# Performance work log

Measured on AMD Instinct MI355X. Metric: run time of the kernel, lower is better.

The kernel has to match this reference:

```python
import jax, jax.numpy as jnp
import numpy as np

B, S, D = 2, 2048, 2048
NH, NKV = 32, 8
HD = D // NH          # 64
NREP = NH // NKV      # 4


def _rope(x, cos, sin):
    # x: [B, S, H, HD]; cos/sin: [S, HD//2]
    x2 = x.reshape(*x.shape[:-1], HD // 2, 2)
    x0, x1 = x2[..., 0], x2[..., 1]
    c = cos[None, :, None, :]
    s = sin[None, :, None, :]
    r0 = x0 * c - x1 * s
    r1 = x0 * s + x1 * c
    return jnp.stack([r0, r1], axis=-1).reshape(x.shape)


def setup_inputs() -> dict:
    key = jax.random.key(0)
    ks = jax.random.split(key, 5)
    x = jax.random.normal(ks[0], (B, S, D), dtype=jnp.float32)
    wq = jax.random.normal(ks[1], (D, NH * HD), dtype=jnp.float32) * (D ** -0.5)
    wk = jax.random.normal(ks[2], (D, NKV * HD), dtype=jnp.float32) * (D ** -0.5)
    wv = jax.random.normal(ks[3], (D, NKV * HD), dtype=jnp.float32) * (D ** -0.5)
    wo = jax.random.normal(ks[4], (NH * HD, D), dtype=jnp.float32) * (D ** -0.5)
    # standard RoPE frequencies: theta = 10000^(-2i/HD)
    inv_freq = 1.0 / (10000.0 ** (np.arange(0, HD, 2, dtype=np.float32) / HD))
    angles = np.arange(S, dtype=np.float32)[:, None] * inv_freq[None, :]  # [S, HD/2]
    freqs_cos = jnp.asarray(np.cos(angles))
    freqs_sin = jnp.asarray(np.sin(angles))
    return {"x": x, "freqs_cos": freqs_cos, "freqs_sin": freqs_sin,
            "wq": wq, "wk": wk, "wv": wv, "wo": wo}


def reference(x, freqs_cos, freqs_sin, wq, wk, wv, wo):
    b, s, _ = x.shape
    xq = (x @ wq).reshape(b, s, NH, HD)
    xk = (x @ wk).reshape(b, s, NKV, HD)
    xv = (x @ wv).reshape(b, s, NKV, HD)
    xq = _rope(xq, freqs_cos, freqs_sin)
    xk = _rope(xk, freqs_cos, freqs_sin)
    # GQA repeat_kv: expand kv heads to NH
    keys = jnp.repeat(xk, NREP, axis=2)    # [B, S, NH, HD]
    values = jnp.repeat(xv, NREP, axis=2)
    scores = jnp.einsum('bqhd,bkhd->bhqk', xq, keys) / jnp.sqrt(jnp.float32(HD))
    causal = jnp.tril(jnp.ones((s, s), dtype=bool))
    scores = jnp.where(causal[None, None], scores, -jnp.inf)
    attn = jax.nn.softmax(scores.astype(jnp.float32), axis=-1).astype(xq.dtype)
    out = jnp.einsum('bhqk,bkhd->bqhd', attn, values).reshape(b, s, NH * HD)
    return out @ wo
```

## Files before the change

### kernel.cpp

```cpp
#include <hip/hip_runtime.h>
#include <hip/hip_bf16.h>

#define S_LEN 2048
#define DMODEL 2048
#define N_H 32
#define N_KV 8
#define H_D 64
#define ROWS 4096
#define QKV_LD 3072

typedef __bf16 bf16x8 __attribute__((ext_vector_type(8)));
typedef float f32x4 __attribute__((ext_vector_type(4)));

static __device__ __forceinline__ unsigned short f2bf(float f) {
  unsigned int u = __float_as_uint(f);
  u += 0x7FFFu + ((u >> 16) & 1u);
  return (unsigned short)(u >> 16);
}
static __device__ __forceinline__ float bf2f(unsigned short s) {
  return __uint_as_float((unsigned int)s << 16);
}

static __device__ __forceinline__ void async16(const void* g, void* l) {
  __builtin_amdgcn_global_load_lds(
      (const __attribute__((address_space(1))) unsigned int*)g,
      (__attribute__((address_space(3))) unsigned int*)l, 16, 0, 0);
}

__global__ __launch_bounds__(256) void cvt_bf16_k(
    const float* __restrict__ in, unsigned short* __restrict__ out) {
  const size_t i = ((size_t)blockIdx.x * 256 + threadIdx.x) * 8;
  const float4 a = *(const float4*)&in[i];
  const float4 b = *(const float4*)&in[i + 4];
  union { unsigned short u[8]; uint4 v; } p;
  p.u[0] = f2bf(a.x); p.u[1] = f2bf(a.y); p.u[2] = f2bf(a.z); p.u[3] = f2bf(a.w);
  p.u[4] = f2bf(b.x); p.u[5] = f2bf(b.y); p.u[6] = f2bf(b.z); p.u[7] = f2bf(b.w);
  *(uint4*)&out[i] = p.v;
}

__global__ __launch_bounds__(256) void prep_all_k(
    const float* __restrict__ x, const float* __restrict__ wq,
    const float* __restrict__ wk, const float* __restrict__ wv,
    const float* __restrict__ wo, unsigned short* __restrict__ xb,
    unsigned short* __restrict__ wqkvT, unsigned short* __restrict__ woT) {
  const int z = blockIdx.z;
  if (z == 4) {
    const size_t i =
        (((size_t)blockIdx.y * 64 + blockIdx.x) * 256 + threadIdx.x) * 8;
    const float4 a = *(const float4*)&x[i];
    const float4 b = *(const float4*)&x[i + 4];
    union { unsigned short u[8]; uint4 v; } p;
    p.u[0] = f2bf(a.x); p.u[1] = f2bf(a.y); p.u[2] = f2bf(a.z); p.u[3] = f2bf(a.w);
    p.u[4] = f2bf(b.x); p.u[5] = f2bf(b.y); p.u[6] = f2bf(b.z); p.u[7] = f2bf(b.w);
    *(uint4*)&xb[i] = p.v;
    return;
  }
  const float* in;
  unsigned short* out;
  int C;
  if (z == 0)      { in = wq; out = wqkvT;                  C = 2048; }
  else if (z == 1) { in = wk; out = wqkvT + 2048ull * 2048; C = 512;  }
  else if (z == 2) { in = wv; out = wqkvT + 2560ull * 2048; C = 512;  }
  else             { in = wo; out = woT;                    C = 2048; }
  if (blockIdx.x * 32 >= C) return;

  __shared__ unsigned short tile[32][33];
  const int tx = threadIdx.x & 31;
  const int ty = threadIdx.x >> 5;
  const int r0 = blockIdx.y * 32;
  const int c0 = blockIdx.x * 32;
#pragma unroll
  for (int i = 0; i < 32; i += 8)
    tile[ty + i][tx] = f2bf(in[(size_t)(r0 + ty + i) * C + c0 + tx]);
  __syncthreads();
#pragma unroll
  for (int i = 0; i < 32; i += 8)
    out[(size_t)(c0 + ty + i) * 2048 + r0 + tx] = tile[tx][ty + i];
}

#define SCALE_LOG2E 0.18033688011112042f

__global__ __launch_bounds__(256) void rope_vt_k(
    unsigned short* __restrict__ qkv, unsigned short* __restrict__ vT,
    const float* __restrict__ fc, const float* __restrict__ fs) {
  const int blk = blockIdx.x;
  if (blk < 20480) {
    const int PQ = ROWS * N_H * (H_D / 2);
    const int PK = ROWS * N_KV * (H_D / 2);
    const int idx = blk * 256 + threadIdx.x;
    if (idx >= PQ + PK) return;
    unsigned short* base;
    float c, sn;
    bool isq;
    if (idx < PQ) {
      const int i = idx & 31;
      const int h = (idx >> 5) & 31;
      const int row = idx >> 10;
      const int s = row & (S_LEN - 1);
      c = fc[s * 32 + i];
      sn = fs[s * 32 + i];
      base = qkv + (size_t)row * QKV_LD + h * H_D + 2 * i;
      isq = true;
    } else {
      const int p = idx - PQ;
      const int i = p & 31;
      const int h = (p >> 5) & 7;
      const int row = p >> 8;
      const int s = row & (S_LEN - 1);
      c = fc[s * 32 + i];
      sn = fs[s * 32 + i];
      base = qkv + (size_t)row * QKV_LD + 2048 + h * H_D + 2 * i;
      isq = false;
    }
    const float x0 = bf2f(base[0]);
    const float x1 = bf2f(base[1]);
    const float sc = isq ? SCALE_LOG2E : 1.0f;
    base[0] = f2bf((x0 * c - x1 * sn) * sc);
    base[1] = f2bf((x0 * sn + x1 * c) * sc);
  } else {
    __shared__ unsigned short tile[32][33];
    const int t = blk - 20480;
    const int bx = t & 15;
    const int by = t >> 4;
    const unsigned short* in = qkv + 2560;
    const int tx = threadIdx.x & 31;
    const int ty = threadIdx.x >> 5;
    const int r0 = by * 32;
    const int c0 = bx * 32;
#pragma unroll
    for (int i = 0; i < 32; i += 8)
      tile[ty + i][tx] = in[(size_t)(r0 + ty + i) * QKV_LD + c0 + tx];
    __syncthreads();
#pragma unroll
    for (int i = 0; i < 32; i += 8)
      vT[(size_t)(c0 + ty + i) * ROWS + r0 + tx] = tile[tx][ty + i];
  }
}

template <int STORE_BF16>
__global__ __launch_bounds__(256) void gemm_bt_k(
    const unsigned short* __restrict__ A, const unsigned short* __restrict__ BT,
    void* __restrict__ Cp, int M, int N, int K, int lda) {
  __shared__ __align__(16) unsigned short As[128 * 32];
  __shared__ __align__(16) unsigned short Bs[128 * 32];
  const int tid = threadIdx.x;
  const int wave = tid >> 6;
  const int lane = tid & 63;
  const int quad = lane >> 4;
  const int l16 = lane & 15;
  const int m0 = blockIdx.x * 128;
  const int n0 = blockIdx.y * 128;
  const int wm = (wave >> 1) * 64;
  const int wn = (wave & 1) * 64;
  const int rsub = lane >> 2;
  const int coff = (lane & 3) * 8;
  f32x4 acc[4][4] = {};

  for (int kt = 0; kt < K; kt += 32) {
    __syncthreads();
#pragma unroll
    for (int t = 0; t < 2; t++) {
      const int row = wave * 32 + t * 16 + rsub;
      async16(&A[(size_t)(m0 + row) * lda + kt + coff],
              &As[(wave * 32 + t * 16) * 32]);
      async16(&BT[(size_t)(n0 + row) * K + kt + coff],
              &Bs[(wave * 32 + t * 16) * 32]);
    }
    __syncthreads();
    bf16x8 af[4], bfr[4];
#pragma unroll
    for (int i = 0; i < 4; i++)
      af[i] = *(const bf16x8*)&As[(wm + i * 16 + l16) * 32 + quad * 8];
#pragma unroll
    for (int j = 0; j < 4; j++)
      bfr[j] = *(const bf16x8*)&Bs[(wn + j * 16 + l16) * 32 + quad * 8];
#pragma unroll
    for (int i = 0; i < 4; i++)
#pragma unroll
      for (int j = 0; j < 4; j++)
        acc[i][j] =
            __builtin_amdgcn_mfma_f32_16x16x32_bf16(af[i], bfr[j], acc[i][j], 0, 0, 0);
  }

#pragma unroll
  for (int i = 0; i < 4; i++) {
#pragma unroll
    for (int e = 0; e < 4; e++) {
      const int mrow = m0 + wm + i * 16 + quad * 4 + e;
#pragma unroll
      for (int j = 0; j < 4; j++) {
        const int ncol = n0 + wn + j * 16 + l16;
        const float val = acc[i][j][e];
        if (STORE_BF16) {
          ((unsigned short*)Cp)[(size_t)mrow * N + ncol] = f2bf(val);
        } else {
          ((float*)Cp)[(size_t)mrow * N + ncol] = val;
        }
      }
    }
  }
}

template <int AF32, int STORE_BF16>
__global__ __launch_bounds__(256) void gemm_k(
    const void* __restrict__ Ap, const float* __restrict__ B,
    void* __restrict__ Cp, int M, int N, int K) {
  constexpr int LDP = 40;
  __shared__ __align__(16) unsigned short As[128 * LDP];
  __shared__ __align__(16) unsigned short Bs[128 * LDP];
  const int tid = threadIdx.x;
  const int wave = tid >> 6;
  const int lane = tid & 63;
  const int quad = lane >> 4;
  const int l16 = lane & 15;
  const int m0 = blockIdx.x * 128;
  const int n0 = blockIdx.y * 128;
  const int wm = (wave >> 1) * 64;
  const int wn = (wave & 1) * 64;
  f32x4 acc[4][4] = {};

  for (int kt = 0; kt < K; kt += 32) {
    __syncthreads();
    if (AF32) {
      const float* A = (const float*)Ap;
      for (int c = tid; c < 1024; c += 256) {
        const int r = c >> 3;
        const int cc = (c & 7) << 2;
        const float4 w = *(const float4*)&A[(size_t)(m0 + r) * K + kt + cc];
        union { unsigned short u[4]; uint2 v; } p;
        p.u[0] = f2bf(w.x); p.u[1] = f2bf(w.y);
        p.u[2] = f2bf(w.z); p.u[3] = f2bf(w.w);
        *(uint2*)&As[r * LDP + cc] = p.v;
      }
    } else {
      const unsigned short* A = (const unsigned short*)Ap;
      for (int c = tid; c < 512; c += 256) {
        const int r = c >> 2;
        const int cc = (c & 3) << 3;
        *(uint4*)&As[r * LDP + cc] =
            *(const uint4*)&A[(size_t)(m0 + r) * K + kt + cc];
      }
    }
    for (int c = tid; c < 1024; c += 256) {
      const int kr = c >> 5;
      const int nc = (c & 31) << 2;
      const float4 w = *(const float4*)&B[(size_t)(kt + kr) * N + n0 + nc];
      Bs[(nc + 0) * LDP + kr] = f2bf(w.x);
      Bs[(nc + 1) * LDP + kr] = f2bf(w.y);
      Bs[(nc + 2) * LDP + kr] = f2bf(w.z);
      Bs[(nc + 3) * LDP + kr] = f2bf(w.w);
    }
    __syncthreads();
    bf16x8 af[4], bfr[4];
#pragma unroll
    for (int i = 0; i < 4; i++)
      af[i] = *(const bf16x8*)&As[(wm + i * 16 + l16) * LDP + quad * 8];
#pragma unroll
    for (int j = 0; j < 4; j++)
      bfr[j] = *(const bf16x8*)&Bs[(wn + j * 16 + l16) * LDP + quad * 8];
#pragma unroll
    for (int i = 0; i < 4; i++)
#pragma unroll
      for (int j = 0; j < 4; j++)
        acc[i][j] =
            __builtin_amdgcn_mfma_f32_16x16x32_bf16(af[i], bfr[j], acc[i][j], 0, 0, 0);
  }
#pragma unroll
  for (int i = 0; i < 4; i++) {
#pragma unroll
    for (int e = 0; e < 4; e++) {
      const int mrow = m0 + wm + i * 16 + quad * 4 + e;
#pragma unroll
      for (int j = 0; j < 4; j++) {
        const int ncol = n0 + wn + j * 16 + l16;
        const float val = acc[i][j][e];
        if (STORE_BF16) {
          ((unsigned short*)Cp)[(size_t)mrow * N + ncol] = f2bf(val);
        } else {
          ((float*)Cp)[(size_t)mrow * N + ncol] = val;
        }
      }
    }
  }
}

__global__ __launch_bounds__(256) void rope_k(
    unsigned short* __restrict__ q, unsigned short* __restrict__ kk,
    const float* __restrict__ fc, const float* __restrict__ fs,
    int qstride, int kstride) {
  const int PQ = ROWS * N_H * (H_D / 2);
  const int PK = ROWS * N_KV * (H_D / 2);
  const int idx = blockIdx.x * 256 + threadIdx.x;
  if (idx >= PQ + PK) return;
  unsigned short* base;
  float c, sn;
  if (idx < PQ) {
    const int i = idx & 31;
    const int h = (idx >> 5) & 31;
    const int row = idx >> 10;
    const int s = row & (S_LEN - 1);
    c = fc[s * 32 + i];
    sn = fs[s * 32 + i];
    base = q + (size_t)row * qstride + h * H_D + 2 * i;
  } else {
    const int p = idx - PQ;
    const int i = p & 31;
    const int h = (p >> 5) & 7;
    const int row = p >> 8;
    const int s = row & (S_LEN - 1);
    c = fc[s * 32 + i];
    sn = fs[s * 32 + i];
    base = kk + (size_t)row * kstride + h * H_D + 2 * i;
  }
  const float x0 = bf2f(base[0]);
  const float x1 = bf2f(base[1]);
  base[0] = f2bf(x0 * c - x1 * sn);
  base[1] = f2bf(x0 * sn + x1 * c);
}

__global__ __launch_bounds__(512, 2) void attn_mfma9_k(
    const unsigned short* __restrict__ qkv, const unsigned short* __restrict__ vT,
    unsigned short* __restrict__ ao) {
  const int pair = blockIdx.x, h = blockIdx.y, b = blockIdx.z;
  const int hk = h >> 2;
  const int tid = threadIdx.x;
  const int wave = tid >> 6;
  const int l16 = tid & 15;
  const int quad = (tid & 63) >> 4;
  const int rr = tid >> 3;
  const int dc = (tid & 7) * 8;
  const int rx = (l16 & 7) << 3;
  const int sx = (rr & 7) << 3;

  __shared__ __align__(16) unsigned short Ks[2][64 * 64];
  __shared__ __align__(16) unsigned short Vt[2][64 * 64];
  __shared__ __align__(16) unsigned short Ps[8][32 * 64];

  bf16x8 ones;
#pragma unroll
  for (int j = 0; j < 8; j++) ones[j] = (__bf16)1.0f;

  const size_t kbase =
      (size_t)(b * S_LEN) * QKV_LD + 2048 + hk * H_D + dc;
  const size_t vbase = (size_t)(hk * H_D + rr) * ROWS + b * S_LEN + dc;

  for (int sel = 0; sel < 2; ++sel) {
    const int qb = sel ? (7 - pair) : pair;
    const int row0 = qb * 256;
    const int ktiles = 4 * qb + 4;

    bf16x8 af[2][2];
#pragma unroll
    for (int r = 0; r < 2; r++) {
      const size_t qrow =
          (size_t)(b * S_LEN + row0 + wave * 32 + r * 16 + l16);
#pragma unroll
      for (int c = 0; c < 2; c++)
        af[r][c] =
            *(const bf16x8*)&qkv[qrow * QKV_LD + h * H_D + c * 32 + quad * 8];
    }

    f32x4 o_acc[2][4] = {};
    f32x4 l_acc[2] = {};

    uint4 rk, rv;
    rk = *(const uint4*)&qkv[kbase + (size_t)rr * QKV_LD];
    rv = *(const uint4*)&vT[vbase];
    __syncthreads();
    *(uint4*)&Ks[0][rr * 64 + (dc ^ sx)] = rk;
    *(uint4*)&Vt[0][rr * 64 + (dc ^ sx)] = rv;

    for (int kt = 0; kt < ktiles; kt += 2) {
#pragma unroll
      for (int half = 0; half < 2; ++half) {
        const int kcur = kt + half;
        if (kcur + 1 < ktiles) {
          rk = *(const uint4*)&qkv[kbase +
                                   (size_t)((kcur + 1) * 64 + rr) * QKV_LD];
          rv = *(const uint4*)&vT[vbase + (size_t)(kcur + 1) * 64];
        }
        __syncthreads();

        f32x4 sacc[2][4];
#pragma unroll
        for (int n = 0; n < 4; n++) {
          f32x4 z0 = {}, z1 = {};
#pragma unroll
          for (int c = 0; c < 2; c++) {
            const bf16x8 bk =
                *(const bf16x8*)&Ks[half][(n * 16 + l16) * 64 +
                                          ((c * 32 + quad * 8) ^ rx)];
            z0 = __builtin_amdgcn_mfma_f32_16x16x32_bf16(bk, af[0][c], z0, 0, 0, 0);
            z1 = __builtin_amdgcn_mfma_f32_16x16x32_bf16(bk, af[1][c], z1, 0, 0, 0);
          }
          sacc[0][n] = z0;
          sacc[1][n] = z1;
        }

        const bool maybe_mask = (kcur >= 4 * qb);
        const int krel0 = (kcur - 4 * qb) * 64;
#pragma unroll
        for (int r = 0; r < 2; r++) {
          const int qn = wave * 32 + r * 16 + l16;
          const int prow = (r * 16 + l16) * 64;
#pragma unroll
          for (int n = 0; n < 4; n++) {
            const int kb0 = krel0 + n * 16 + quad * 4;
            float pe[4];
#pragma unroll
            for (int e = 0; e < 4; e++) {
              float v = exp2f(sacc[r][n][e]);
              if (maybe_mask && (kb0 + e > qn)) v = 0.f;
              pe[e] = v;
            }
            uint2 u;
            u.x = __builtin_amdgcn_perm(__float_as_uint(pe[1]),
                                        __float_as_uint(pe[0]), 0x07060302u);
            u.y = __builtin_amdgcn_perm(__float_as_uint(pe[3]),
                                        __float_as_uint(pe[2]), 0x07060302u);
            *(uint2*)&Ps[wave][prow + ((n * 16 + quad * 4) ^ rx)] = u;
          }
        }

        bf16x8 pf[2][2];
#pragma unroll
        for (int r = 0; r < 2; r++)
#pragma unroll
          for (int c = 0; c < 2; c++)
            pf[r][c] = *(const bf16x8*)&Ps[wave][(r * 16 + l16) * 64 +
                                                ((c * 32 + quad * 8) ^ rx)];
#pragma unroll
        for (int c = 0; c < 2; c++) {
          l_acc[0] = __builtin_amdgcn_mfma_f32_16x16x32_bf16(pf[0][c], ones,
                                                             l_acc[0], 0, 0, 0);
          l_acc[1] = __builtin_amdgcn_mfma_f32_16x16x32_bf16(pf[1][c], ones,
                                                             l_acc[1], 0, 0, 0);
        }
#pragma unroll
        for (int n = 0; n < 4; n++)
#pragma unroll
          for (int c = 0; c < 2; c++) {
            const bf16x8 bv =
                *(const bf16x8*)&Vt[half][(n * 16 + l16) * 64 +
                                          ((c * 32 + quad * 8) ^ rx)];
            o_acc[0][n] = __builtin_amdgcn_mfma_f32_16x16x32_bf16(
                pf[0][c], bv, o_acc[0][n], 0, 0, 0);
            o_acc[1][n] = __builtin_amdgcn_mfma_f32_16x16x32_bf16(
                pf[1][c], bv, o_acc[1][n], 0, 0, 0);
          }

        if (kcur + 1 < ktiles) {
          *(uint4*)&Ks[half ^ 1][rr * 64 + (dc ^ sx)] = rk;
          *(uint4*)&Vt[half ^ 1][rr * 64 + (dc ^ sx)] = rv;
        }
      }
    }

#pragma unroll
    for (int r = 0; r < 2; r++)
#pragma unroll
      for (int e = 0; e < 4; e++) {
        const float inv = 1.f / l_acc[r][e];
        const size_t row =
            (size_t)(b * S_LEN + row0 + wave * 32 + r * 16 + quad * 4 + e);
#pragma unroll
        for (int n = 0; n < 4; n++)
          ao[row * QKV_LD + h * H_D + n * 16 + l16] = f2bf(o_acc[r][n][e] * inv);
      }
  }
}

#define LK 72

__global__ __launch_bounds__(256) void attn_mfma_k(
    const unsigned short* __restrict__ q, const unsigned short* __restrict__ k,
    const unsigned short* __restrict__ v, unsigned short* __restrict__ ao) {
  const int qt = blockIdx.x, h = blockIdx.y, b = blockIdx.z;
  const int hk = h >> 2;
  const int tid = threadIdx.x;
  const int wave = tid >> 6;
  const int l16 = tid & 15;
  const int quad = (tid & 63) >> 4;

  __shared__ __align__(16) unsigned short Ks[64 * LK];
  __shared__ __align__(16) unsigned short Vt[64 * LK];
  __shared__ __align__(16) unsigned short Ps[64 * LK];

  bf16x8 af[2];
  {
    const size_t qrow = (size_t)(b * S_LEN + qt * 64 + wave * 16 + l16);
#pragma unroll
    for (int c = 0; c < 2; c++)
      af[c] = *(const bf16x8*)&q[qrow * DMODEL + h * H_D + c * 32 + quad * 8];
  }

  f32x4 o_acc[4] = {};
  float m_i[4], l_i[4];
#pragma unroll
  for (int e = 0; e < 4; e++) { m_i[e] = -INFINITY; l_i[e] = 0.f; }

  for (int kt = 0; kt <= qt; ++kt) {
    const int kb = kt * 64;
    __syncthreads();
    {
      const int kr = tid >> 2;
      const int dc = (tid & 3) * 16;
      const size_t gro = (size_t)(b * S_LEN + kb + kr) * (N_KV * H_D) + hk * H_D + dc;
      *(uint4*)&Ks[kr * LK + dc] = *(const uint4*)&k[gro];
      *(uint4*)&Ks[kr * LK + dc + 8] = *(const uint4*)&k[gro + 8];
      union { unsigned short u[8]; uint4 v; } w0, w1;
      w0.v = *(const uint4*)&v[gro];
      w1.v = *(const uint4*)&v[gro + 8];
#pragma unroll
      for (int j = 0; j < 8; j++) Vt[(dc + j) * LK + kr] = w0.u[j];
#pragma unroll
      for (int j = 0; j < 8; j++) Vt[(dc + 8 + j) * LK + kr] = w1.u[j];
    }
    __syncthreads();

    f32x4 sacc[4];
#pragma unroll
    for (int n = 0; n < 4; n++) {
      f32x4 z = {};
#pragma unroll
      for (int c = 0; c < 2; c++) {
        const bf16x8 bk = *(const bf16x8*)&Ks[(n * 16 + l16) * LK + c * 32 + quad * 8];
        z = __builtin_amdgcn_mfma_f32_16x16x32_bf16(af[c], bk, z, 0, 0, 0);
      }
      sacc[n] = z;
    }

    float p[4][4], mnew[4];
#pragma unroll
    for (int e = 0; e < 4; e++) mnew[e] = m_i[e];
#pragma unroll
    for (int n = 0; n < 4; n++)
#pragma unroll
      for (int e = 0; e < 4; e++) {
        float s = sacc[n][e] * 0.125f;
        if (kt == qt && (n * 16 + l16) > (wave * 16 + quad * 4 + e))
          s = -INFINITY;
        p[n][e] = s;
        mnew[e] = fmaxf(mnew[e], s);
      }
#pragma unroll
    for (int e = 0; e < 4; e++) {
      mnew[e] = fmaxf(mnew[e], __shfl_xor(mnew[e], 1));
      mnew[e] = fmaxf(mnew[e], __shfl_xor(mnew[e], 2));
      mnew[e] = fmaxf(mnew[e], __shfl_xor(mnew[e], 4));
      mnew[e] = fmaxf(mnew[e], __shfl_xor(mnew[e], 8));
      const float alpha = __expf(m_i[e] - mnew[e]);
      m_i[e] = mnew[e];
      l_i[e] *= alpha;
#pragma unroll
      for (int n = 0; n < 4; n++) o_acc[n][e] *= alpha;
    }
#pragma unroll
    for (int n = 0; n < 4; n++)
#pragma unroll
      for (int e = 0; e < 4; e++) {
        const float pe = __expf(p[n][e] - m_i[e]);
        p[n][e] = pe;
        l_i[e] += pe;
      }

#pragma unroll
    for (int n = 0; n < 4; n++)
#pragma unroll
      for (int e = 0; e < 4; e++)
        Ps[(wave * 16 + quad * 4 + e) * LK + n * 16 + l16] = f2bf(p[n][e]);
    __syncthreads();

    bf16x8 pf[2];
#pragma unroll
    for (int c = 0; c < 2; c++)
      pf[c] = *(const bf16x8*)&Ps[(wave * 16 + l16) * LK + c * 32 + quad * 8];
#pragma unroll
    for (int n = 0; n < 4; n++)
#pragma unroll
      for (int c = 0; c < 2; c++) {
        const bf16x8 bv = *(const bf16x8*)&Vt[(n * 16 + l16) * LK + c * 32 + quad * 8];
        o_acc[n] = __builtin_amdgcn_mfma_f32_16x16x32_bf16(pf[c], bv, o_acc[n], 0, 0, 0);
      }
  }

#pragma unroll
  for (int e = 0; e < 4; e++) {
    l_i[e] += __shfl_xor(l_i[e], 1);
    l_i[e] += __shfl_xor(l_i[e], 2);
    l_i[e] += __shfl_xor(l_i[e], 4);
    l_i[e] += __shfl_xor(l_i[e], 8);
    const float inv = 1.f / l_i[e];
    const size_t row = (size_t)(b * S_LEN + qt * 64 + wave * 16 + quad * 4 + e);
#pragma unroll
    for (int n = 0; n < 4; n++)
      ao[row * DMODEL + h * H_D + n * 16 + l16] = f2bf(o_acc[n][e] * inv);
  }
}

extern "C" void kernel_launch(void* const* d_in, const int* in_sizes, int n_in,
                              void* d_out, int out_size, void* d_ws, size_t ws_size,
                              hipStream_t stream) {
  const float* x = (const float*)d_in[0];
  const float* fc = (const float*)d_in[1];
  const float* fs = (const float*)d_in[2];
  const float* wq = (const float*)d_in[3];
  const float* wk = (const float*)d_in[4];
  const float* wv = (const float*)d_in[5];
  const float* wo = (const float*)d_in[6];

  char* ws = (char*)d_ws;
  const dim3 b256(256);

  if (ws_size >= (64ull << 20)) {
    unsigned short* qkv = (unsigned short*)(ws);
    unsigned short* xb = (unsigned short*)(ws + (24ull << 20));
    unsigned short* wqkvT = (unsigned short*)(ws + (40ull << 20));
    unsigned short* woT = (unsigned short*)(ws + (52ull << 20));
    unsigned short* vT = (unsigned short*)(ws + (60ull << 20));

    prep_all_k<<<dim3(64, 64, 5), b256, 0, stream>>>(x, wq, wk, wv, wo, xb,
                                                     wqkvT, woT);

    gemm_bt_k<1><<<dim3(32, 24), b256, 0, stream>>>(xb, wqkvT, qkv, 4096, 3072,
                                                    2048, 2048);

    rope_vt_k<<<dim3(20480 + 2048), b256, 0, stream>>>(qkv, vT, fc, fs);

    attn_mfma9_k<<<dim3(4, N_H, 2), dim3(512), 0, stream>>>(qkv, vT, qkv);

    gemm_bt_k<0><<<dim3(32, 16), b256, 0, stream>>>(qkv, woT, d_out, 4096, 2048,
                                                    2048, QKV_LD);
  } else {
    unsigned short* q = (unsigned short*)(ws);
    unsigned short* k = (unsigned short*)(ws + (16ull << 20));
    unsigned short* v = (unsigned short*)(ws + (20ull << 20));
    unsigned short* xb = (unsigned short*)(ws + (24ull << 20));
    const bool have_xb = ws_size >= (40ull << 20);

    if (have_xb) {
      cvt_bf16_k<<<dim3(ROWS * DMODEL / (256 * 8)), b256, 0, stream>>>(x, xb);
      gemm_k<0, 1><<<dim3(32, 16), b256, 0, stream>>>(xb, wq, q, 4096, 2048, 2048);
      gemm_k<0, 1><<<dim3(32, 4), b256, 0, stream>>>(xb, wk, k, 4096, 512, 2048);
      gemm_k<0, 1><<<dim3(32, 4), b256, 0, stream>>>(xb, wv, v, 4096, 512, 2048);
    } else {
      gemm_k<1, 1><<<dim3(32, 16), b256, 0, stream>>>(x, wq, q, 4096, 2048, 2048);
      gemm_k<1, 1><<<dim3(32, 4), b256, 0, stream>>>(x, wk, k, 4096, 512, 2048);
      gemm_k<1, 1><<<dim3(32, 4), b256, 0, stream>>>(x, wv, v, 4096, 512, 2048);
    }

    rope_k<<<dim3(20480), b256, 0, stream>>>(q, k, fc, fs, N_H * H_D, N_KV * H_D);
    attn_mfma_k<<<dim3(S_LEN / 64, N_H, 2), b256, 0, stream>>>(q, k, v, q);
    gemm_k<0, 0><<<dim3(32, 16), b256, 0, stream>>>(q, wo, d_out, 4096, 2048, 2048);
  }
}
```

Before: 324.4 us.

## Split attention key tiles across two wave groups with LDS reduction

The attention kernel now processes 128-row query blocks with two groups of four waves. Each group handles alternate 64-key tiles from the same query rows, and the partial outputs and row sums are combined through shared memory at the end. The grid doubles to 8 pairs per head and the launch bound is raised to 4 blocks per CU, aiming for more parallelism and better load balance in the causal loop. In exchange it adds an extra cross-group reduction and more barriers, and an odd-length tail is avoided only because the tile count is always even.

```diff
diff --git a/kernel.cpp b/kernel.cpp
--- a/kernel.cpp
+++ b/kernel.cpp
@@ -318,13 +318,16 @@
   base[1] = f2bf(x0 * sn + x1 * c);
 }
 
-__global__ __launch_bounds__(512, 2) void attn_mfma9_k(
+__global__ __launch_bounds__(512, 4) void attn_mfma10_k(
     const unsigned short* __restrict__ qkv, const unsigned short* __restrict__ vT,
     unsigned short* __restrict__ ao) {
   const int pair = blockIdx.x, h = blockIdx.y, b = blockIdx.z;
   const int hk = h >> 2;
   const int tid = threadIdx.x;
   const int wave = tid >> 6;
+  const int g = wave >> 2;
+  const int w4 = wave & 3;
+  const int lane = tid & 63;
   const int l16 = tid & 15;
   const int quad = (tid & 63) >> 4;
   const int rr = tid >> 3;
@@ -336,6 +339,12 @@
   __shared__ __align__(16) unsigned short Vt[2][64 * 64];
   __shared__ __align__(16) unsigned short Ps[8][32 * 64];
 
+  const unsigned short* Kb = &Ks[g][0];
+  const unsigned short* Vb = &Vt[g][0];
+
+  f32x4* Ored = (f32x4*)&Ps[0][0];
+  f32x4* Lred = (f32x4*)&Ks[0][0];
+
   bf16x8 ones;
 #pragma unroll
   for (int j = 0; j < 8; j++) ones[j] = (__bf16)1.0f;
@@ -345,15 +354,15 @@
   const size_t vbase = (size_t)(hk * H_D + rr) * ROWS + b * S_LEN + dc;
 
   for (int sel = 0; sel < 2; ++sel) {
-    const int qb = sel ? (7 - pair) : pair;
-    const int row0 = qb * 256;
-    const int ktiles = 4 * qb + 4;
+    const int qb = sel ? (15 - pair) : pair;
+    const int row0 = qb * 128;
+    const int ktiles = 2 * qb + 2;
 
     bf16x8 af[2][2];
 #pragma unroll
     for (int r = 0; r < 2; r++) {
       const size_t qrow =
-          (size_t)(b * S_LEN + row0 + wave * 32 + r * 16 + l16);
+          (size_t)(b * S_LEN + row0 + w4 * 32 + r * 16 + l16);
 #pragma unroll
       for (int c = 0; c < 2; c++)
         af[r][c] =
@@ -363,110 +372,134 @@
     f32x4 o_acc[2][4] = {};
     f32x4 l_acc[2] = {};
 
-    uint4 rk, rv;
-    rk = *(const uint4*)&qkv[kbase + (size_t)rr * QKV_LD];
-    rv = *(const uint4*)&vT[vbase];
-    __syncthreads();
-    *(uint4*)&Ks[0][rr * 64 + (dc ^ sx)] = rk;
-    *(uint4*)&Vt[0][rr * 64 + (dc ^ sx)] = rv;
+    uint4 rk0, rk1, rv0, rv1;
+    rk0 = *(const uint4*)&qkv[kbase + (size_t)(0 * 64 + rr) * QKV_LD];
+    rk1 = *(const uint4*)&qkv[kbase + (size_t)(1 * 64 + rr) * QKV_LD];
+    rv0 = *(const uint4*)&vT[vbase + (size_t)0 * 64];
+    rv1 = *(const uint4*)&vT[vbase + (size_t)1 * 64];
+    __syncthreads();
+    *(uint4*)&Ks[0][rr * 64 + (dc ^ sx)] = rk0;
+    *(uint4*)&Ks[1][rr * 64 + (dc ^ sx)] = rk1;
+    *(uint4*)&Vt[0][rr * 64 + (dc ^ sx)] = rv0;
+    *(uint4*)&Vt[1][rr * 64 + (dc ^ sx)] = rv1;
 
     for (int kt = 0; kt < ktiles; kt += 2) {
-#pragma unroll
-      for (int half = 0; half < 2; ++half) {
-        const int kcur = kt + half;
-        if (kcur + 1 < ktiles) {
-          rk = *(const uint4*)&qkv[kbase +
-                                   (size_t)((kcur + 1) * 64 + rr) * QKV_LD];
-          rv = *(const uint4*)&vT[vbase + (size_t)(kcur + 1) * 64];
+      if (kt + 2 < ktiles) {
+        rk0 = *(const uint4*)&qkv[kbase + (size_t)((kt + 2) * 64 + rr) * QKV_LD];
+        rk1 = *(const uint4*)&qkv[kbase + (size_t)((kt + 3) * 64 + rr) * QKV_LD];
+        rv0 = *(const uint4*)&vT[vbase + (size_t)(kt + 2) * 64];
+        rv1 = *(const uint4*)&vT[vbase + (size_t)(kt + 3) * 64];
+      }
+      __syncthreads();
+
+      const int kcur = kt + g;
+
+      f32x4 sacc[2][4];
+#pragma unroll
+      for (int n = 0; n < 4; n++) {
+        f32x4 z0 = {}, z1 = {};
+#pragma unroll
+        for (int c = 0; c < 2; c++) {
+          const bf16x8 bk = *(const bf16x8*)&Kb[(n * 16 + l16) * 64 +
+                                               ((c * 32 + quad * 8) ^ rx)];
+          z0 = __builtin_amdgcn_mfma_f32_16x16x32_bf16(bk, af[0][c], z0, 0, 0, 0);
+          z1 = __builtin_amdgcn_mfma_f32_16x16x32_bf16(bk, af[1][c], z1, 0, 0, 0);
         }
-        __syncthreads();
-
-        f32x4 sacc[2][4];
+        sacc[0][n] = z0;
+        sacc[1][n] = z1;
+      }
+
+      const bool maybe_mask = (kcur >= 2 * qb);
+      const int krel0 = (kcur - 2 * qb) * 64;
+#pragma unroll
+      for (int r = 0; r < 2; r++) {
+        const int qn = w4 * 32 + r * 16 + l16;
+        const int prow = (r * 16 + l16) * 64;
 #pragma unroll
         for (int n = 0; n < 4; n++) {
-          f32x4 z0 = {}, z1 = {};
-#pragma unroll
-          for (int c = 0; c < 2; c++) {
-            const bf16x8 bk =
-                *(const bf16x8*)&Ks[half][(n * 16 + l16) * 64 +
-                                          ((c * 32 + quad * 8) ^ rx)];
-            z0 = __builtin_amdgcn_mfma_f32_16x16x32_bf16(bk, af[0][c], z0, 0, 0, 0);
-            z1 = __builtin_amdgcn_mfma_f32_16x16x32_bf16(bk, af[1][c], z1, 0, 0, 0);
+          const int kb0 = krel0 + n * 16 + quad * 4;
+          float pe[4];
+#pragma unroll
+          for (int e = 0; e < 4; e++) {
+            float v = exp2f(sacc[r][n][e]);
+            if (maybe_mask && (kb0 + e > qn)) v = 0.f;
+            pe[e] = v;
           }
-          sacc[0][n] = z0;
-          sacc[1][n] = z1;
+          uint2 u;
+          u.x = __builtin_amdgcn_perm(__float_as_uint(pe[1]),
+                                      __float_as_uint(pe[0]), 0x07060302u);
+          u.y = __builtin_amdgcn_perm(__float_as_uint(pe[3]),
+                                      __float_as_uint(pe[2]), 0x07060302u);
+          *(uint2*)&Ps[wave][prow + ((n * 16 + quad * 4) ^ rx)] = u;
         }
-
-        const bool maybe_mask = (kcur >= 4 * qb);
-        const int krel0 = (kcur - 4 * qb) * 64;
-#pragma unroll
-        for (int r = 0; r < 2; r++) {
-          const int qn = wave * 32 + r * 16 + l16;
-          const int prow = (r * 16 + l16) * 64;
-#pragma unroll
-          for (int n = 0; n < 4; n++) {
-            const int kb0 = krel0 + n * 16 + quad * 4;
-            float pe[4];
-#pragma unroll
-            for (int e = 0; e < 4; e++) {
-              float v = exp2f(sacc[r][n][e]);
-              if (maybe_mask && (kb0 + e > qn)) v = 0.f;
-              pe[e] = v;
-            }
-            uint2 u;
-            u.x = __builtin_amdgcn_perm(__float_as_uint(pe[1]),
-                                        __float_as_uint(pe[0]), 0x07060302u);
-            u.y = __builtin_amdgcn_perm(__float_as_uint(pe[3]),
-                                        __float_as_uint(pe[2]), 0x07060302u);
-            *(uint2*)&Ps[wave][prow + ((n * 16 + quad * 4) ^ rx)] = u;
-          }
+      }
+
+      bf16x8 pf[2][2];
+#pragma unroll
+      for (int r = 0; r < 2; r++)
+#pragma unroll
+        for (int c = 0; c < 2; c++)
+          pf[r][c] = *(const bf16x8*)&Ps[wave][(r * 16 + l16) * 64 +
+                                              ((c * 32 + quad * 8) ^ rx)];
+#pragma unroll
+      for (int c = 0; c < 2; c++) {
+        l_acc[0] = __builtin_amdgcn_mfma_f32_16x16x32_bf16(pf[0][c], ones,
+                                                           l_acc[0], 0, 0, 0);
+        l_acc[1] = __builtin_amdgcn_mfma_f32_16x16x32_bf16(pf[1][c], ones,
+                                                           l_acc[1], 0, 0, 0);
+      }
+#pragma unroll
+      for (int n = 0; n < 4; n++)
+#pragma unroll
+        for (int c = 0; c < 2; c++) {
+          const bf16x8 bv = *(const bf16x8*)&Vb[(n * 16 + l16) * 64 +
+                                               ((c * 32 + quad * 8) ^ rx)];
+          o_acc[0][n] = __builtin_amdgcn_mfma_f32_16x16x32_bf16(
+              pf[0][c], bv, o_acc[0][n], 0, 0, 0);
+          o_acc[1][n] = __builtin_amdgcn_mfma_f32_16x16x32_bf16(
+              pf[1][c], bv, o_acc[1][n], 0, 0, 0);
         }
 
-        bf16x8 pf[2][2];
-#pragma unroll
-        for (int r = 0; r < 2; r++)
-#pragma unroll
-          for (int c = 0; c < 2; c++)
-            pf[r][c] = *(const bf16x8*)&Ps[wave][(r * 16 + l16) * 64 +
-                                                ((c * 32 + quad * 8) ^ rx)];
-#pragma unroll
-        for (int c = 0; c < 2; c++) {
-          l_acc[0] = __builtin_amdgcn_mfma_f32_16x16x32_bf16(pf[0][c], ones,
-                                                             l_acc[0], 0, 0, 0);
-          l_acc[1] = __builtin_amdgcn_mfma_f32_16x16x32_bf16(pf[1][c], ones,
-                                                             l_acc[1], 0, 0, 0);
+      __syncthreads();
+      if (kt + 2 < ktiles) {
+        *(uint4*)&Ks[0][rr * 64 + (dc ^ sx)] = rk0;
+        *(uint4*)&Ks[1][rr * 64 + (dc ^ sx)] = rk1;
+        *(uint4*)&Vt[0][rr * 64 + (dc ^ sx)] = rv0;
+        *(uint4*)&Vt[1][rr * 64 + (dc ^ sx)] = rv1;
+      }
+    }
+
+    if (g == 1) {
+#pragma unroll
+      for (int r = 0; r < 2; r++) {
+#pragma unroll
+        for (int n = 0; n < 4; n++)
+          Ored[(w4 * 8 + r * 4 + n) * 64 + lane] = o_acc[r][n];
+        Lred[(w4 * 2 + r) * 64 + lane] = l_acc[r];
+      }
+    }
+    __syncthreads();
+    if (g == 0) {
+#pragma unroll
+      for (int r = 0; r < 2; r++) {
+#pragma unroll
+        for (int n = 0; n < 4; n++)
+          o_acc[r][n] += Ored[(w4 * 8 + r * 4 + n) * 64 + lane];
+        l_acc[r] += Lred[(w4 * 2 + r) * 64 + lane];
+      }
+#pragma unroll
+      for (int r = 0; r < 2; r++)
+#pragma unroll
+        for (int e = 0; e < 4; e++) {
+          const float inv = 1.f / l_acc[r][e];
+          const size_t row =
+              (size_t)(b * S_LEN + row0 + w4 * 32 + r * 16 + quad * 4 + e);
+#pragma unroll
+          for (int n = 0; n < 4; n++)
+            ao[row * QKV_LD + h * H_D + n * 16 + l16] =
+                f2bf(o_acc[r][n][e] * inv);
         }
-#pragma unroll
-        for (int n = 0; n < 4; n++)
-#pragma unroll
-          for (int c = 0; c < 2; c++) {
-            const bf16x8 bv =
-                *(const bf16x8*)&Vt[half][(n * 16 + l16) * 64 +
-                                          ((c * 32 + quad * 8) ^ rx)];
-            o_acc[0][n] = __builtin_amdgcn_mfma_f32_16x16x32_bf16(
-                pf[0][c], bv, o_acc[0][n], 0, 0, 0);
-            o_acc[1][n] = __builtin_amdgcn_mfma_f32_16x16x32_bf16(
-                pf[1][c], bv, o_acc[1][n], 0, 0, 0);
-          }
-
-        if (kcur + 1 < ktiles) {
-          *(uint4*)&Ks[half ^ 1][rr * 64 + (dc ^ sx)] = rk;
-          *(uint4*)&Vt[half ^ 1][rr * 64 + (dc ^ sx)] = rv;
-        }
-      }
-    }
-
-#pragma unroll
-    for (int r = 0; r < 2; r++)
-#pragma unroll
-      for (int e = 0; e < 4; e++) {
-        const float inv = 1.f / l_acc[r][e];
-        const size_t row =
-            (size_t)(b * S_LEN + row0 + wave * 32 + r * 16 + quad * 4 + e);
-#pragma unroll
-        for (int n = 0; n < 4; n++)
-          ao[row * QKV_LD + h * H_D + n * 16 + l16] = f2bf(o_acc[r][n][e] * inv);
-      }
+    }
   }
 }
 
@@ -627,7 +660,7 @@
 
     rope_vt_k<<<dim3(20480 + 2048), b256, 0, stream>>>(qkv, vT, fc, fs);
 
-    attn_mfma9_k<<<dim3(4, N_H, 2), dim3(512), 0, stream>>>(qkv, vT, qkv);
+    attn_mfma10_k<<<dim3(8, N_H, 2), dim3(512), 0, stream>>>(qkv, vT, qkv);
 
     gemm_bt_k<0><<<dim3(32, 16), b256, 0, stream>>>(qkv, woT, d_out, 4096, 2048,
                                                     2048, QKV_LD);
```

New measurement: 333.7 us. 1.03x slower.
